# Kernel optimization log

Measured on AMD Instinct MI355X. Metric: run time of the kernel, lower is better.

## Reference

```python
import jax, jax.numpy as jnp
import numpy as np

NUM_SPEAKERS = 8  # static speaker vocabulary size for the per-speaker state


def setup_inputs() -> dict:
    key = jax.random.key(0)
    ks = jax.random.split(key, 6)
    B, T, L, D = 8, 256, 64, 768
    input_ids = jax.random.randint(ks[0], (B, T, L), 0, 32000, dtype=jnp.int32)
    speaker_ids = jax.random.randint(ks[1], (B, T), 0, NUM_SPEAKERS, dtype=jnp.int32)
    token_embeddings = jax.random.normal(ks[2], (B, T, L, D), dtype=jnp.float32)
    edu_embeddings = jax.random.normal(ks[3], (B, T, D), dtype=jnp.float32)
    # nn.Linear(d, d, bias=False) weights, torch layout [out, in]
    Wk = jax.random.normal(ks[4], (D, D), dtype=jnp.float32) / np.sqrt(D)
    Wv = jax.random.normal(ks[5], (D, D), dtype=jnp.float32) / np.sqrt(D)
    return {"input_ids": input_ids, "speaker_ids": speaker_ids,
            "token_embeddings": token_embeddings, "edu_embeddings": edu_embeddings,
            "Wk": Wk, "Wv": Wv}


def reference(input_ids, speaker_ids, token_embeddings, edu_embeddings, Wk, Wv):
    B, T, L = input_ids.shape
    D = edu_embeddings.shape[-1]
    # projections (torch Linear: x @ W.T)
    k = jnp.einsum('btd,ed->bte', edu_embeddings, Wk)  # [B,T,D]
    v = jnp.einsum('btd,ed->bte', edu_embeddings, Wv)  # [B,T,D]

    b_idx = jnp.arange(B)

    def step(state, inp):
        # state: per-speaker running kv_sum, [B, S, D, D]
        k_t, v_t, spk_t, tok_t = inp  # [B,D], [B,D], [B], [B,L,D]
        kv = k_t[:, :, None] * v_t[:, None, :]           # outer(k, v): [B,D,D]
        state = state.at[b_idx, spk_t].add(kv)           # segmented accumulate
        M = state[b_idx, spk_t]                          # [B,D,D] current speaker memory
        out_t = tok_t + jnp.einsum('bij,blj->bli', M, tok_t)
        return state, out_t

    state0 = jnp.zeros((B, NUM_SPEAKERS, D, D), dtype=token_embeddings.dtype)
    xs = (jnp.swapaxes(k, 0, 1), jnp.swapaxes(v, 0, 1),
          jnp.swapaxes(speaker_ids, 0, 1), jnp.swapaxes(token_embeddings, 0, 1))
    _, out = jax.lax.scan(step, state0, xs)              # out: [T,B,L,D]
    return jnp.swapaxes(out, 0, 1)                       # [B,T,L,D]
```

## Files before the change

kernel.cpp:

```cpp
#include <hip/hip_runtime.h>
#include <hip/hip_bf16.h>

#define NB 8
#define NT 256
#define NL 64
#define ND 768

typedef __attribute__((ext_vector_type(4))) float f32x4;
typedef __attribute__((ext_vector_type(8))) short bf16x8;

__device__ __forceinline__ short f2bs(float f) {
    __hip_bfloat16 h = __float2bfloat16(f);
    return *reinterpret_cast<short*>(&h);
}
__device__ __forceinline__ unsigned pack2(float a, float b) {
    return (unsigned)(ushort)f2bs(a) | ((unsigned)(ushort)f2bs(b) << 16);
}

__global__ __launch_bounds__(256, 4) void projm_kernel(
    const float* __restrict__ E, const float* __restrict__ Wk,
    const float* __restrict__ Wv, float* __restrict__ kws,
    float* __restrict__ vws)
{
    const float* W = (blockIdx.z == 0) ? Wk : Wv;
    float* O       = (blockIdx.z == 0) ? kws : vws;
    const int m0 = blockIdx.x * 64;
    const int e0 = blockIdx.y * 64;

    __shared__ ushort Et[2][4096];
    __shared__ ushort Wt[2][4096];

    const int tid = threadIdx.x;
    const int lane = tid & 63, w = tid >> 6;
    const int fr = lane & 15;
    const int fq = lane >> 4;
    const int row2 = tid >> 4;
    const int c4   = tid & 15;

    const f32x4 z4 = {0.f, 0.f, 0.f, 0.f};
    f32x4 acc[4];
    #pragma unroll
    for (int et = 0; et < 4; ++et) acc[et] = z4;

    float4 ea[2][4], wa[2][4];
    #pragma unroll
    for (int p = 0; p < 4; ++p) {
        ea[0][p] = *(const float4*)(E + (size_t)(m0 + row2 + 16 * p) * ND + c4 * 4);
        wa[0][p] = *(const float4*)(W + (size_t)(e0 + row2 + 16 * p) * ND + c4 * 4);
    }

    #pragma unroll
    for (int dt = 0; dt < 12; ++dt) {
        const int cur = dt & 1, nxt = cur ^ 1;
        #pragma unroll
        for (int p = 0; p < 4; ++p) {
            const int r = row2 + 16 * p;
            const int uidx = (r * 64 + c4 * 4) ^ ((r & 7) << 3);
            uint2 te; te.x = pack2(ea[cur][p].x, ea[cur][p].y); te.y = pack2(ea[cur][p].z, ea[cur][p].w);
            uint2 tw; tw.x = pack2(wa[cur][p].x, wa[cur][p].y); tw.y = pack2(wa[cur][p].z, wa[cur][p].w);
            *(uint2*)&Et[cur][uidx] = te;
            *(uint2*)&Wt[cur][uidx] = tw;
        }
        if (dt < 11) {
            const int c0 = (dt + 1) * 64 + c4 * 4;
            #pragma unroll
            for (int p = 0; p < 4; ++p) {
                ea[nxt][p] = *(const float4*)(E + (size_t)(m0 + row2 + 16 * p) * ND + c0);
                wa[nxt][p] = *(const float4*)(W + (size_t)(e0 + row2 + 16 * p) * ND + c0);
            }
        }
        __syncthreads();
        const int brow = w * 16 + fr;
        const int bsw  = (brow & 7) << 3;
        #pragma unroll
        for (int ks = 0; ks < 2; ++ks) {
            bf16x8 bv = *(const bf16x8*)&Et[cur][(brow * 64 + ks * 32 + fq * 8) ^ bsw];
            #pragma unroll
            for (int et = 0; et < 4; ++et) {
                const int arow = et * 16 + fr;
                bf16x8 af = *(const bf16x8*)&Wt[cur][(arow * 64 + ks * 32 + fq * 8) ^ ((arow & 7) << 3)];
                acc[et] = __builtin_amdgcn_mfma_f32_16x16x32_bf16(af, bv, acc[et], 0, 0, 0);
            }
        }
    }

    float* ob = O + (size_t)(m0 + w * 16 + fr) * ND + e0 + fq * 4;
    #pragma unroll
    for (int et = 0; et < 4; ++et)
        *(f32x4*)(ob + et * 16) = acc[et];
}

__global__ __launch_bounds__(256, 3) void s_kernel(
    const int* __restrict__ spk, const float* __restrict__ tok,
    const float* __restrict__ vws, ushort* __restrict__ S_ws, int cap)
{
    __shared__ int mlist[NT];
    __shared__ int wavecnt[4];
    __shared__ ushort At[2][4096];
    __shared__ ushort Vt[2][4096];
    __shared__ ushort Sb[4096];

    const int bt  = blockIdx.x;
    const int b   = bt >> 8;
    const int t   = bt & 255;
    const int tid = threadIdx.x;

    const int tgt = spk[b * NT + t];
    int my = -1;
    if (tid <= t) my = spk[b * NT + tid];
    const bool match = (tid <= t) && (my == tgt);
    unsigned long long bal = __ballot(match);
    const int lane = tid & 63, w = tid >> 6;
    if (lane == 0) wavecnt[w] = __popcll(bal);
    __syncthreads();
    int off = 0;
    #pragma unroll
    for (int ww = 0; ww < 4; ++ww) if (ww < w) off += wavecnt[ww];
    const int n = wavecnt[0] + wavecnt[1] + wavecnt[2] + wavecnt[3];
    const int before = __popcll(bal & ((1ull << lane) - 1ull));
    if (match) mlist[off + before] = tid;
    __syncthreads();

    const int fr = lane & 15;
    const int fq = lane >> 4;
    const int rb = tid >> 4;
    const int c4 = tid & 15;

    const size_t tokbase = (size_t)bt * NL * ND;
    const float* vbase = vws + (size_t)b * NT * ND;
    const f32x4 z4 = {0.f, 0.f, 0.f, 0.f};

    const int nchunk = min((n + 63) >> 6, cap);
    for (int cc = 0; cc < nchunk; ++cc) {
        const int j0 = cc * 64;
        int gr[4];
        #pragma unroll
        for (int p = 0; p < 4; ++p) {
            const int jj = j0 + rb + 16 * p;
            gr[p] = mlist[jj < n ? jj : n - 1];
        }
        float4 ta[4], va[4];
        #pragma unroll
        for (int p = 0; p < 4; ++p) {
            ta[p] = *(const float4*)(tok + tokbase + (size_t)(rb + 16 * p) * ND + c4 * 4);
            va[p] = *(const float4*)(vbase + (size_t)gr[p] * ND + c4 * 4);
        }
        f32x4 accS[4];
        #pragma unroll
        for (int jt = 0; jt < 4; ++jt) accS[jt] = z4;

        for (int dt = 0; dt < 12; ++dt) {
            const int cur = dt & 1;
            #pragma unroll
            for (int p = 0; p < 4; ++p) {
                const int row = rb + 16 * p;
                const int uidx = (row * 64 + c4 * 4) ^ ((row & 7) << 3);
                uint2 tw; tw.x = pack2(ta[p].x, ta[p].y); tw.y = pack2(ta[p].z, ta[p].w);
                uint2 vw; vw.x = pack2(va[p].x, va[p].y); vw.y = pack2(va[p].z, va[p].w);
                *(uint2*)&At[cur][uidx] = tw;
                *(uint2*)&Vt[cur][uidx] = vw;
            }
            if (dt < 11) {
                const int c0 = (dt + 1) * 64 + c4 * 4;
                #pragma unroll
                for (int p = 0; p < 4; ++p) {
                    ta[p] = *(const float4*)(tok + tokbase + (size_t)(rb + 16 * p) * ND + c0);
                    va[p] = *(const float4*)(vbase + (size_t)gr[p] * ND + c0);
                }
            }
            __syncthreads();
            const int arow = w * 16 + fr;
            #pragma unroll
            for (int ks = 0; ks < 2; ++ks) {
                bf16x8 af = *(const bf16x8*)&At[cur][(arow * 64 + ks * 32 + fq * 8) ^ ((arow & 7) << 3)];
                #pragma unroll
                for (int jt = 0; jt < 4; ++jt) {
                    const int brow = jt * 16 + fr;
                    bf16x8 bv = *(const bf16x8*)&Vt[cur][(brow * 64 + ks * 32 + fq * 8) ^ ((brow & 7) << 3)];
                    accS[jt] = __builtin_amdgcn_mfma_f32_16x16x32_bf16(af, bv, accS[jt], 0, 0, 0);
                }
            }
        }

        #pragma unroll
        for (int jt = 0; jt < 4; ++jt) {
            #pragma unroll
            for (int i = 0; i < 4; ++i) {
                const int r = w * 16 + fq * 4 + i;
                const int c = jt * 16 + fr;
                Sb[(r * 64 + c) ^ ((r & 7) << 3)] = (ushort)f2bs(accS[jt][i]);
            }
        }
        __syncthreads();
        ushort* dst = S_ws + ((size_t)bt * 4 + cc) * 4096;
        #pragma unroll
        for (int g = 0; g < 2; ++g) {
            const int wsg = g * 256 + tid;
            const int r = wsg >> 3, c8 = wsg & 7;
            *(f32x4*)&dst[(size_t)wsg * 8] = *(const f32x4*)&Sb[(r * 64 + c8 * 8) ^ ((r & 7) << 3)];
        }
        __syncthreads();
    }
}

__global__ __launch_bounds__(256, 4) void b_kernel(
    const int* __restrict__ spk, const float* __restrict__ tok,
    const float* __restrict__ kws, const ushort* __restrict__ S_ws,
    float* __restrict__ out, int cap)
{
    __shared__ int mlist[NT];
    __shared__ int wavecnt[4];
    __shared__ ushort Sb[4096];
    __shared__ ushort kT[8192];

    const int bt  = blockIdx.x;
    const int st  = blockIdx.y;
    const int b   = bt >> 8;
    const int t   = bt & 255;
    const int tid = threadIdx.x;
    const int lane = tid & 63, w = tid >> 6;
    const int fr = lane & 15;
    const int fq = lane >> 4;

    const size_t tokbase = (size_t)bt * NL * ND;

    f32x4 acco[8];
    {
        const float* rbp = tok + tokbase + (size_t)(w * 16 + fr) * ND + st * 128 + fq * 4;
        #pragma unroll
        for (int ct = 0; ct < 8; ++ct)
            acco[ct] = *(const f32x4*)(rbp + ct * 16);
    }

    const int tgt = spk[b * NT + t];
    int my = -1;
    if (tid <= t) my = spk[b * NT + tid];
    const bool match = (tid <= t) && (my == tgt);
    unsigned long long bal = __ballot(match);
    if (lane == 0) wavecnt[w] = __popcll(bal);
    __syncthreads();
    int off = 0;
    #pragma unroll
    for (int ww = 0; ww < 4; ++ww) if (ww < w) off += wavecnt[ww];
    const int n = wavecnt[0] + wavecnt[1] + wavecnt[2] + wavecnt[3];
    const int before = __popcll(bal & ((1ull << lane) - 1ull));
    if (match) mlist[off + before] = tid;
    __syncthreads();

    const int jr = tid >> 2;
    const int q  = tid & 3;
    const float* kbase = kws + (size_t)b * NT * ND;
    const f32x4 zf = {0.f, 0.f, 0.f, 0.f};

    const int nchunk = min((n + 63) >> 6, cap);
    for (int cc = 0; cc < nchunk; ++cc) {
        const int j0 = cc * 64;
        const ushort* src = S_ws + ((size_t)bt * 4 + cc) * 4096;
        f32x4 sv0 = *(const f32x4*)&src[(size_t)tid * 8];
        f32x4 sv1 = *(const f32x4*)&src[(size_t)(256 + tid) * 8];
        const int jj = j0 + jr;
        const int g = (jj < n) ? mlist[jj] : -1;
        f32x4 kreg[8];
        #pragma unroll
        for (int p = 0; p < 8; ++p)
            kreg[p] = (g >= 0)
                ? *(const f32x4*)(kbase + (size_t)g * ND + st * 128 + (q + 4 * p) * 4)
                : zf;

        if (cc > 0) __syncthreads();
        {
            int wsg = tid, r = wsg >> 3, c8 = wsg & 7;
            *(f32x4*)&Sb[(r * 64 + c8 * 8) ^ ((r & 7) << 3)] = sv0;
            wsg = 256 + tid; r = wsg >> 3; c8 = wsg & 7;
            *(f32x4*)&Sb[(r * 64 + c8 * 8) ^ ((r & 7) << 3)] = sv1;
        }
        #pragma unroll
        for (int p = 0; p < 8; ++p) {
            #pragma unroll
            for (int e = 0; e < 4; ++e) {
                const int dc = (q + 4 * p) * 4 + e;
                kT[(dc * 64 + jr) ^ ((dc & 7) << 3)] = (ushort)f2bs(kreg[p][e]);
            }
        }
        __syncthreads();

        const int srow = w * 16 + fr;
        const int ssw  = (srow & 7) << 3;
        #pragma unroll
        for (int ks = 0; ks < 2; ++ks) {
            bf16x8 bv = *(const bf16x8*)&Sb[(srow * 64 + ks * 32 + fq * 8) ^ ssw];
            #pragma unroll
            for (int ct = 0; ct < 8; ++ct) {
                const int drow = ct * 16 + fr;
                bf16x8 af = *(const bf16x8*)&kT[(drow * 64 + ks * 32 + fq * 8) ^ ((drow & 7) << 3)];
                acco[ct] = __builtin_amdgcn_mfma_f32_16x16x32_bf16(af, bv, acco[ct], 0, 0, 0);
            }
        }
    }

    float* ob = out + tokbase + (size_t)(w * 16 + fr) * ND + st * 128 + fq * 4;
    #pragma unroll
    for (int ct = 0; ct < 8; ++ct)
        *(f32x4*)(ob + ct * 16) = acco[ct];
}

extern "C" void kernel_launch(void* const* d_in, const int* in_sizes, int n_in,
                              void* d_out, int out_size, void* d_ws, size_t ws_size,
                              hipStream_t stream) {
    const int*   spk = (const int*)d_in[1];
    const float* tok = (const float*)d_in[2];
    const float* edu = (const float*)d_in[3];
    const float* Wk  = (const float*)d_in[4];
    const float* Wv  = (const float*)d_in[5];

    const size_t kv_floats = (size_t)NB * NT * ND;
    float* kws = (float*)d_ws;
    float* vws = kws + kv_floats;
    ushort* S_ws = (ushort*)(vws + kv_floats);
    const size_t s_bytes_per_chunkset = (size_t)NB * NT * 4096ull * 2ull;
    size_t avail = (ws_size > 2 * kv_floats * 4) ? (ws_size - 2 * kv_floats * 4) : 0;
    int cap = (int)(avail / s_bytes_per_chunkset);
    if (cap > 4) cap = 4;
    if (cap < 1) cap = 1;
    float* outp = (float*)d_out;

    projm_kernel<<<dim3(2048 / 64, ND / 64, 2), 256, 0, stream>>>(edu, Wk, Wv, kws, vws);
    s_kernel<<<NB * NT, 256, 0, stream>>>(spk, tok, vws, S_ws, cap);
    b_kernel<<<dim3(NB * NT, 6), 256, 0, stream>>>(spk, tok, kws, S_ws, outp, cap);
}
```

Before: 324.0 us.

## Fuse score and output kernels, keeping S tile in LDS

Merges s_kernel and b_kernel into one kernel per (b,t) block. Each 64x64 bf16 S chunk stays in shared memory and is consumed right away, and the output is built by looping over six 128-column slabs inside the block. This drops the S workspace round trip through global memory and one launch. In exchange, b_kernel's 6-way grid split is gone, so each block has less parallelism. Chunks after the first read back and rewrite the output from global memory, and LDS is aliased between At and kT.

```diff
diff --git a/kernel.cpp b/kernel.cpp
--- a/kernel.cpp
+++ b/kernel.cpp
@@ -90,15 +90,20 @@
         *(f32x4*)(ob + et * 16) = acc[et];
 }
 
-__global__ __launch_bounds__(256, 3) void s_kernel(
+__global__ __launch_bounds__(256, 3) void fused_kernel(
     const int* __restrict__ spk, const float* __restrict__ tok,
-    const float* __restrict__ vws, ushort* __restrict__ S_ws, int cap)
+    const float* __restrict__ kws, const float* __restrict__ vws,
+    float* __restrict__ out)
 {
     __shared__ int mlist[NT];
     __shared__ int wavecnt[4];
-    __shared__ ushort At[2][4096];
+    __shared__ ushort U[8192];
     __shared__ ushort Vt[2][4096];
     __shared__ ushort Sb[4096];
+
+    ushort* At0 = U;
+    ushort* At1 = U + 4096;
+    ushort* kT  = U;
 
     const int bt  = blockIdx.x;
     const int b   = bt >> 8;
@@ -125,14 +130,18 @@
     const int fq = lane >> 4;
     const int rb = tid >> 4;
     const int c4 = tid & 15;
+    const int jr = tid >> 2;
+    const int q  = tid & 3;
 
     const size_t tokbase = (size_t)bt * NL * ND;
     const float* vbase = vws + (size_t)b * NT * ND;
+    const float* kbase = kws + (size_t)b * NT * ND;
     const f32x4 z4 = {0.f, 0.f, 0.f, 0.f};
 
-    const int nchunk = min((n + 63) >> 6, cap);
+    const int nchunk = min((n + 63) >> 6, 4);
     for (int cc = 0; cc < nchunk; ++cc) {
         const int j0 = cc * 64;
+
         int gr[4];
         #pragma unroll
         for (int p = 0; p < 4; ++p) {
@@ -151,13 +160,14 @@
 
         for (int dt = 0; dt < 12; ++dt) {
             const int cur = dt & 1;
+            ushort* Atc = cur ? At1 : At0;
             #pragma unroll
             for (int p = 0; p < 4; ++p) {
                 const int row = rb + 16 * p;
                 const int uidx = (row * 64 + c4 * 4) ^ ((row & 7) << 3);
                 uint2 tw; tw.x = pack2(ta[p].x, ta[p].y); tw.y = pack2(ta[p].z, ta[p].w);
                 uint2 vw; vw.x = pack2(va[p].x, va[p].y); vw.y = pack2(va[p].z, va[p].w);
-                *(uint2*)&At[cur][uidx] = tw;
+                *(uint2*)&Atc[uidx] = tw;
                 *(uint2*)&Vt[cur][uidx] = vw;
             }
             if (dt < 11) {
@@ -172,7 +182,7 @@
             const int arow = w * 16 + fr;
             #pragma unroll
             for (int ks = 0; ks < 2; ++ks) {
-                bf16x8 af = *(const bf16x8*)&At[cur][(arow * 64 + ks * 32 + fq * 8) ^ ((arow & 7) << 3)];
+                bf16x8 af = *(const bf16x8*)&Atc[(arow * 64 + ks * 32 + fq * 8) ^ ((arow & 7) << 3)];
                 #pragma unroll
                 for (int jt = 0; jt < 4; ++jt) {
                     const int brow = jt * 16 + fr;
@@ -192,116 +202,65 @@
             }
         }
         __syncthreads();
-        ushort* dst = S_ws + ((size_t)bt * 4 + cc) * 4096;
-        #pragma unroll
-        for (int g = 0; g < 2; ++g) {
-            const int wsg = g * 256 + tid;
-            const int r = wsg >> 3, c8 = wsg & 7;
-            *(f32x4*)&dst[(size_t)wsg * 8] = *(const f32x4*)&Sb[(r * 64 + c8 * 8) ^ ((r & 7) << 3)];
+
+        const int jj = j0 + jr;
+        const int g = (jj < n) ? mlist[jj] : -1;
+        const float* bp = (cc == 0) ? (tok + tokbase) : (const float*)(out + tokbase);
+        const f32x4 zf = {0.f, 0.f, 0.f, 0.f};
+
+        f32x4 kreg[8];
+        #pragma unroll
+        for (int p = 0; p < 8; ++p)
+            kreg[p] = (g >= 0)
+                ? *(const f32x4*)(kbase + (size_t)g * ND + (q + 4 * p) * 4)
+                : zf;
+
+        for (int st = 0; st < 6; ++st) {
+            if (st > 0) __syncthreads();
+            #pragma unroll
+            for (int p = 0; p < 8; ++p) {
+                #pragma unroll
+                for (int e = 0; e < 4; ++e) {
+                    const int dc = (q + 4 * p) * 4 + e;
+                    kT[(dc * 64 + jr) ^ ((dc & 7) << 3)] = (ushort)f2bs(kreg[p][e]);
+                }
+            }
+            f32x4 acco[8];
+            {
+                const float* rbp = bp + (size_t)(w * 16 + fr) * ND + st * 128 + fq * 4;
+                #pragma unroll
+                for (int ct = 0; ct < 8; ++ct)
+                    acco[ct] = *(const f32x4*)(rbp + ct * 16);
+            }
+            if (st < 5) {
+                const int c0 = (st + 1) * 128;
+                #pragma unroll
+                for (int p = 0; p < 8; ++p)
+                    kreg[p] = (g >= 0)
+                        ? *(const f32x4*)(kbase + (size_t)g * ND + c0 + (q + 4 * p) * 4)
+                        : zf;
+            }
+            __syncthreads();
+
+            const int srow = w * 16 + fr;
+            const int ssw  = (srow & 7) << 3;
+            #pragma unroll
+            for (int ks = 0; ks < 2; ++ks) {
+                bf16x8 bv = *(const bf16x8*)&Sb[(srow * 64 + ks * 32 + fq * 8) ^ ssw];
+                #pragma unroll
+                for (int ct = 0; ct < 8; ++ct) {
+                    const int drow = ct * 16 + fr;
+                    bf16x8 af = *(const bf16x8*)&kT[(drow * 64 + ks * 32 + fq * 8) ^ ((drow & 7) << 3)];
+                    acco[ct] = __builtin_amdgcn_mfma_f32_16x16x32_bf16(af, bv, acco[ct], 0, 0, 0);
+                }
+            }
+            float* ob = out + tokbase + (size_t)(w * 16 + fr) * ND + st * 128 + fq * 4;
+            #pragma unroll
+            for (int ct = 0; ct < 8; ++ct)
+                *(f32x4*)(ob + ct * 16) = acco[ct];
         }
         __syncthreads();
     }
-}
-
-__global__ __launch_bounds__(256, 4) void b_kernel(
-    const int* __restrict__ spk, const float* __restrict__ tok,
-    const float* __restrict__ kws, const ushort* __restrict__ S_ws,
-    float* __restrict__ out, int cap)
-{
-    __shared__ int mlist[NT];
-    __shared__ int wavecnt[4];
-    __shared__ ushort Sb[4096];
-    __shared__ ushort kT[8192];
-
-    const int bt  = blockIdx.x;
-    const int st  = blockIdx.y;
-    const int b   = bt >> 8;
-    const int t   = bt & 255;
-    const int tid = threadIdx.x;
-    const int lane = tid & 63, w = tid >> 6;
-    const int fr = lane & 15;
-    const int fq = lane >> 4;
-
-    const size_t tokbase = (size_t)bt * NL * ND;
-
-    f32x4 acco[8];
-    {
-        const float* rbp = tok + tokbase + (size_t)(w * 16 + fr) * ND + st * 128 + fq * 4;
-        #pragma unroll
-        for (int ct = 0; ct < 8; ++ct)
-            acco[ct] = *(const f32x4*)(rbp + ct * 16);
-    }
-
-    const int tgt = spk[b * NT + t];
-    int my = -1;
-    if (tid <= t) my = spk[b * NT + tid];
-    const bool match = (tid <= t) && (my == tgt);
-    unsigned long long bal = __ballot(match);
-    if (lane == 0) wavecnt[w] = __popcll(bal);
-    __syncthreads();
-    int off = 0;
-    #pragma unroll
-    for (int ww = 0; ww < 4; ++ww) if (ww < w) off += wavecnt[ww];
-    const int n = wavecnt[0] + wavecnt[1] + wavecnt[2] + wavecnt[3];
-    const int before = __popcll(bal & ((1ull << lane) - 1ull));
-    if (match) mlist[off + before] = tid;
-    __syncthreads();
-
-    const int jr = tid >> 2;
-    const int q  = tid & 3;
-    const float* kbase = kws + (size_t)b * NT * ND;
-    const f32x4 zf = {0.f, 0.f, 0.f, 0.f};
-
-    const int nchunk = min((n + 63) >> 6, cap);
-    for (int cc = 0; cc < nchunk; ++cc) {
-        const int j0 = cc * 64;
-        const ushort* src = S_ws + ((size_t)bt * 4 + cc) * 4096;
-        f32x4 sv0 = *(const f32x4*)&src[(size_t)tid * 8];
-        f32x4 sv1 = *(const f32x4*)&src[(size_t)(256 + tid) * 8];
-        const int jj = j0 + jr;
-        const int g = (jj < n) ? mlist[jj] : -1;
-        f32x4 kreg[8];
-        #pragma unroll
-        for (int p = 0; p < 8; ++p)
-            kreg[p] = (g >= 0)
-                ? *(const f32x4*)(kbase + (size_t)g * ND + st * 128 + (q + 4 * p) * 4)
-                : zf;
-
-        if (cc > 0) __syncthreads();
-        {
-            int wsg = tid, r = wsg >> 3, c8 = wsg & 7;
-            *(f32x4*)&Sb[(r * 64 + c8 * 8) ^ ((r & 7) << 3)] = sv0;
-            wsg = 256 + tid; r = wsg >> 3; c8 = wsg & 7;
-            *(f32x4*)&Sb[(r * 64 + c8 * 8) ^ ((r & 7) << 3)] = sv1;
-        }
-        #pragma unroll
-        for (int p = 0; p < 8; ++p) {
-            #pragma unroll
-            for (int e = 0; e < 4; ++e) {
-                const int dc = (q + 4 * p) * 4 + e;
-                kT[(dc * 64 + jr) ^ ((dc & 7) << 3)] = (ushort)f2bs(kreg[p][e]);
-            }
-        }
-        __syncthreads();
-
-        const int srow = w * 16 + fr;
-        const int ssw  = (srow & 7) << 3;
-        #pragma unroll
-        for (int ks = 0; ks < 2; ++ks) {
-            bf16x8 bv = *(const bf16x8*)&Sb[(srow * 64 + ks * 32 + fq * 8) ^ ssw];
-            #pragma unroll
-            for (int ct = 0; ct < 8; ++ct) {
-                const int drow = ct * 16 + fr;
-                bf16x8 af = *(const bf16x8*)&kT[(drow * 64 + ks * 32 + fq * 8) ^ ((drow & 7) << 3)];
-                acco[ct] = __builtin_amdgcn_mfma_f32_16x16x32_bf16(af, bv, acco[ct], 0, 0, 0);
-            }
-        }
-    }
-
-    float* ob = out + tokbase + (size_t)(w * 16 + fr) * ND + st * 128 + fq * 4;
-    #pragma unroll
-    for (int ct = 0; ct < 8; ++ct)
-        *(f32x4*)(ob + ct * 16) = acco[ct];
 }
 
 extern "C" void kernel_launch(void* const* d_in, const int* in_sizes, int n_in,
@@ -316,15 +275,8 @@
     const size_t kv_floats = (size_t)NB * NT * ND;
     float* kws = (float*)d_ws;
     float* vws = kws + kv_floats;
-    ushort* S_ws = (ushort*)(vws + kv_floats);
-    const size_t s_bytes_per_chunkset = (size_t)NB * NT * 4096ull * 2ull;
-    size_t avail = (ws_size > 2 * kv_floats * 4) ? (ws_size - 2 * kv_floats * 4) : 0;
-    int cap = (int)(avail / s_bytes_per_chunkset);
-    if (cap > 4) cap = 4;
-    if (cap < 1) cap = 1;
     float* outp = (float*)d_out;
 
     projm_kernel<<<dim3(2048 / 64, ND / 64, 2), 256, 0, stream>>>(edu, Wk, Wv, kws, vws);
-    s_kernel<<<NB * NT, 256, 0, stream>>>(spk, tok, vws, S_ws, cap);
-    b_kernel<<<dim3(NB * NT, 6), 256, 0, stream>>>(spk, tok, kws, S_ws, outp, cap);
-}
+    fused_kernel<<<NB * NT, 256, 0, stream>>>(spk, tok, kws, vws, outp);
+}
```

After: 315.8 us. 2.5% less time.
